# Optimization experiments

Hardware: AMD Instinct MI355X
Metric: run time of the kernel (lower is better)

Reference implementation:

```python
import jax, jax.numpy as jnp
import numpy as np

THRESH_FACTOR = 0.7


def ternarize(w):
    # w: [in_features, out_features]; per-row (dim 0) delta/alpha stats
    n = w.shape[1]
    abs_w = jnp.abs(w)
    delta = (THRESH_FACTOR / n) * abs_w.sum(axis=1, keepdims=True)  # [in, 1]
    mask = abs_w > delta
    count = mask.sum(axis=1, keepdims=True).astype(w.dtype)
    alpha = jnp.where(mask, abs_w, 0).sum(axis=1, keepdims=True) / count  # [in, 1]
    tern = jnp.where(w > delta, 1.0, jnp.where(w < -delta, -1.0, 0.0)).astype(w.dtype)
    return tern * alpha


def setup_inputs() -> dict:
    key = jax.random.key(0)
    k1, k2, k3 = jax.random.split(key, 3)
    B, IN, OUT = 8192, 4096, 4096
    x = jax.random.normal(k1, (B, IN), dtype=jnp.float32)
    # kaiming-uniform-ish then clamp to [-1, 1] as in the module
    bound_w = float(np.sqrt(6.0 / ((1.0 + 5.0) * IN)))
    weights = jax.random.uniform(k2, (IN, OUT), minval=-bound_w, maxval=bound_w, dtype=jnp.float32)
    weights = jnp.clip(weights, -1.0, 1.0)
    bound_b = 1.0 / float(np.sqrt(IN))
    bias = jax.random.uniform(k3, (OUT,), minval=-bound_b, maxval=bound_b, dtype=jnp.float32)
    return {"x": x, "weights": weights, "bias": bias}


def reference(x, weights, bias):
    w_t = ternarize(weights)
    return jnp.matmul(x, w_t) + bias
```

## Files before the change

### kernel.cpp

```cpp
#include <hip/hip_runtime.h>
#include <stdint.h>
#include <stddef.h>

#define IN_F 4096
#define OUT_F 4096

typedef int i32x4 __attribute__((ext_vector_type(4)));
typedef float f32x4 __attribute__((ext_vector_type(4)));


__device__ static inline void async16(const void* g, void* l) {
    __builtin_amdgcn_global_load_lds(
        (const __attribute__((address_space(1))) unsigned int*)g,
        (__attribute__((address_space(3))) unsigned int*)l,
        16, 0, 0);
}

__device__ static inline double wred_d(double v) {
#pragma unroll
    for (int o = 32; o > 0; o >>= 1) v += __shfl_down(v, o, 64);
    return v;
}

__device__ static inline int wred_i(int v) {
#pragma unroll
    for (int o = 32; o > 0; o >>= 1) v += __shfl_down(v, o, 64);
    return v;
}

__device__ static inline float wred_max(float v) {
#pragma unroll
    for (int o = 32; o > 0; o >>= 1) v = fmaxf(v, __shfl_down(v, o, 64));
    return v;
}


__global__ __launch_bounds__(256) void rowstats_tern_kernel(
    const float* __restrict__ w,
    float* __restrict__ alpha_o,
    int8_t* __restrict__ T) {
    __shared__ float rowbuf[OUT_F];
    __shared__ double sh_s[4], sh_m[4];
    __shared__ int sh_c[4];
    const int row = blockIdx.x;
    const int t = threadIdx.x;
    const int lane = t & 63, wv = t >> 6;
    const float4* wr = (const float4*)(w + (size_t)row * OUT_F);

    double s = 0.0;
#pragma unroll
    for (int it = 0; it < 4; ++it) {
        float4 v = wr[t + it * 256];
        ((float4*)rowbuf)[t + it * 256] = v;
        s += (double)fabsf(v.x) + (double)fabsf(v.y) +
             (double)fabsf(v.z) + (double)fabsf(v.w);
    }
    double sw = wred_d(s);
    if (lane == 0) sh_s[wv] = sw;
    __syncthreads();
    const double delta = (sh_s[0] + sh_s[1] + sh_s[2] + sh_s[3]) *
                         (0.7 / (double)OUT_F);

    int8_t* trow = T + (size_t)row * OUT_F;
    double ms = 0.0;
    int cnt = 0;
#pragma unroll
    for (int k = 0; k < 16; ++k) {
        float v = rowbuf[k * 256 + t];
        double a = (double)fabsf(v);
        if (a > delta) { ms += a; ++cnt; }
        int8_t q = 0;
        if ((double)v > delta)       q = 1;
        else if ((double)v < -delta) q = -1;
        trow[k * 256 + t] = q;
    }
    double msw = wred_d(ms);
    int cw = wred_i(cnt);
    if (lane == 0) { sh_m[wv] = msw; sh_c[wv] = cw; }
    __syncthreads();
    if (t == 0) {
        double mtot = sh_m[0] + sh_m[1] + sh_m[2] + sh_m[3];
        int ctot = sh_c[0] + sh_c[1] + sh_c[2] + sh_c[3];
        alpha_o[row] = (float)(mtot / (double)ctot);
    }
}


__global__ __launch_bounds__(256) void transpose_i8_kernel(
    const int8_t* __restrict__ T,
    int8_t* __restrict__ Tt) {
    __shared__ int8_t lds[64][72];
    const int t = threadIdx.x;
    const int i0 = blockIdx.y * 64;
    const int j0 = blockIdx.x * 64;

#pragma unroll
    for (int it = 0; it < 4; ++it) {
        int idx = it * 256 + t;
        int r = idx >> 4;
        int c4 = idx & 15;
        uchar4 v = *(const uchar4*)(T + (size_t)(i0 + r) * OUT_F + j0 + c4 * 4);
        lds[c4 * 4 + 0][r] = (int8_t)v.x;
        lds[c4 * 4 + 1][r] = (int8_t)v.y;
        lds[c4 * 4 + 2][r] = (int8_t)v.z;
        lds[c4 * 4 + 3][r] = (int8_t)v.w;
    }
    __syncthreads();
#pragma unroll
    for (int it = 0; it < 2; ++it) {
        int idx = it * 256 + t;
        int rr = idx >> 3;
        int cc = idx & 7;
        unsigned long long v = *(const unsigned long long*)&lds[rr][cc * 8];
        *(unsigned long long*)(Tt + (size_t)(j0 + rr) * IN_F + i0 + cc * 8) = v;
    }
}


__global__ __launch_bounds__(256) void xquant_kernel(
    const float* __restrict__ x,
    const float* __restrict__ alpha,
    int8_t* __restrict__ xq,
    float* __restrict__ scale_o) {
    __shared__ float rowbuf[IN_F];
    __shared__ float sh_mx[4];
    const int row = blockIdx.x;
    const int t = threadIdx.x;
    const int lane = t & 63, wv = t >> 6;
    const float4* xr = (const float4*)(x + (size_t)row * IN_F);
    const float4* ar = (const float4*)alpha;

    float mx = 0.0f;
#pragma unroll
    for (int it = 0; it < 4; ++it) {
        float4 v = xr[t + it * 256];
        float4 a = ar[t + it * 256];
        v.x *= a.x; v.y *= a.y; v.z *= a.z; v.w *= a.w;
        ((float4*)rowbuf)[t + it * 256] = v;
        mx = fmaxf(mx, fmaxf(fmaxf(fabsf(v.x), fabsf(v.y)),
                             fmaxf(fabsf(v.z), fabsf(v.w))));
    }
    float mw = wred_max(mx);
    if (lane == 0) sh_mx[wv] = mw;
    __syncthreads();
    const float rmax = fmaxf(fmaxf(sh_mx[0], sh_mx[1]), fmaxf(sh_mx[2], sh_mx[3]));
    const float inv = (rmax > 0.0f) ? (127.0f / rmax) : 0.0f;

    int8_t* qrow = xq + (size_t)row * IN_F;
#pragma unroll
    for (int k = 0; k < 16; ++k) {
        float v = rowbuf[k * 256 + t];
        qrow[k * 256 + t] = (int8_t)__float2int_rn(v * inv);
    }
    if (t == 0) scale_o[row] = (rmax > 0.0f) ? (rmax / 127.0f) : 1.0f;
}


__global__ __launch_bounds__(256) void gemm_i8_kernel(
    const int8_t* __restrict__ Xq,
    const int8_t* __restrict__ Tq,
    const float* __restrict__ scale,
    const float* __restrict__ bias,
    float* __restrict__ out) {
    __shared__ __align__(16) int8_t lds_a[128 * 64];
    __shared__ __align__(16) int8_t lds_b[128 * 64];
    const int K = IN_F;
    const int t = threadIdx.x;
    const int lane = t & 63;
    const int wave = t >> 6;
    const int m0 = blockIdx.y * 128;
    const int n0 = blockIdx.x * 128;

    const int r0 = t >> 2;
    const int cb = (t & 3) << 4;
    const int8_t* gA0 = Xq + (size_t)(m0 + r0) * K + cb;
    const int8_t* gA1 = Xq + (size_t)(m0 + r0 + 64) * K + cb;
    const int8_t* gB0 = Tq + (size_t)(n0 + r0) * K + cb;
    const int8_t* gB1 = Tq + (size_t)(n0 + r0 + 64) * K + cb;
    char* lA0 = (char*)lds_a + t * 16;
    char* lA1 = (char*)lds_a + t * 16 + 4096;
    char* lB0 = (char*)lds_b + t * 16;
    char* lB1 = (char*)lds_b + t * 16 + 4096;

    i32x4 acc[4][4];
#pragma unroll
    for (int i = 0; i < 4; ++i)
#pragma unroll
        for (int j = 0; j < 4; ++j)
#pragma unroll
            for (int r = 0; r < 4; ++r) acc[i][j][r] = 0;

    const int q16 = (lane >> 4) << 4;
    const int lm = lane & 15;
    const int wm = (wave >> 1) << 6;
    const int wn = (wave & 1) << 6;
    const int8_t* pa = lds_a + (wm + lm) * 64 + q16;
    const int8_t* pb = lds_b + (wn + lm) * 64 + q16;

    for (int k0 = 0; k0 < K; k0 += 64) {
        async16(gA0 + k0, lA0);
        async16(gA1 + k0, lA1);
        async16(gB0 + k0, lB0);
        async16(gB1 + k0, lB1);
        __syncthreads();
        i32x4 af[4], bf[4];
#pragma unroll
        for (int i = 0; i < 4; ++i) {
            af[i] = *(const i32x4*)(pa + i * 16 * 64);
            bf[i] = *(const i32x4*)(pb + i * 16 * 64);
        }
#pragma unroll
        for (int i = 0; i < 4; ++i)
#pragma unroll
            for (int j = 0; j < 4; ++j)
                acc[i][j] = __builtin_amdgcn_mfma_i32_16x16x64_i8(
                    af[i], bf[j], acc[i][j], 0, 0, 0);
        __syncthreads();
    }

    const int q4 = (lane >> 4) << 2;
#pragma unroll
    for (int i = 0; i < 4; ++i) {
        float sc[4];
#pragma unroll
        for (int r = 0; r < 4; ++r) sc[r] = scale[m0 + wm + i * 16 + q4 + r];
#pragma unroll
        for (int j = 0; j < 4; ++j) {
            int col = n0 + wn + j * 16 + lm;
            float b = bias[col];
#pragma unroll
            for (int r = 0; r < 4; ++r) {
                int row = m0 + wm + i * 16 + q4 + r;
                out[(size_t)row * OUT_F + col] =
                    (float)acc[i][j][r] * sc[r] + b;
            }
        }
    }
}


extern "C" void kernel_launch(void* const* d_in, const int* in_sizes, int n_in,
                              void* d_out, int out_size, void* d_ws, size_t ws_size,
                              hipStream_t stream) {
    const float* x = (const float*)d_in[0];
    const float* w = (const float*)d_in[1];
    const float* bias = (const float*)d_in[2];
    float* out = (float*)d_out;
    const int B = in_sizes[0] / IN_F;

    char* ws = (char*)d_ws;
    int8_t* Tt = (int8_t*)ws;
    int8_t* T = (int8_t*)(ws + (size_t)16777216);
    int8_t* Xq = (int8_t*)(ws + (size_t)16777216);
    float* alpha = (float*)(ws + (size_t)50331648);
    float* scale = (float*)(ws + (size_t)50331648 + 16384);

    rowstats_tern_kernel<<<IN_F, 256, 0, stream>>>(w, alpha, T);
    transpose_i8_kernel<<<dim3(OUT_F / 64, IN_F / 64), 256, 0, stream>>>(T, Tt);
    xquant_kernel<<<B, 256, 0, stream>>>(x, alpha, Xq, scale);
    gemm_i8_kernel<<<dim3(OUT_F / 128, B / 128), 256, 0, stream>>>(Xq, Tt, scale, bias, out);
}
```

Measured before the change: 441.8 us.

## Rewrite int8 GEMM as 256x256 tile, 8-wave, double-buffered phased pipeline

Replaces the 128x128 single-buffer int8 GEMM with a 256x256-tile, 512-thread kernel. It uses 128KB of dynamic LDS for double buffering, XOR-swizzled LDS layout to avoid bank conflicts, and an 8-phase schedule that interleaves async global->LDS loads with MFMA blocks under s_setprio. It also adds a grid swizzle for L2 locality. The aim is to hide memory latency and raise arithmetic intensity in the dominant GEMM, at the cost of high register/LDS use and hand-managed waitcnt/barrier correctness.

New measurement: 384.9 us. 1.15x faster.

```diff
diff --git a/kernel.cpp b/kernel.cpp
--- a/kernel.cpp
+++ b/kernel.cpp
@@ -156,83 +156,172 @@
 }
 
 
-__global__ __launch_bounds__(256) void gemm_i8_kernel(
+#define GBARRIER() asm volatile("s_barrier" ::: "memory")
+
+#define STAGE(G, GR0, TILE, LBASE, HALF)                                        \
+    do {                                                                        \
+        _Pragma("unroll")                                                       \
+        for (int rr_ = 0; rr_ < 2; ++rr_) {                                     \
+            const int L_ = (HALF) * 1024 + rr_ * 512 + t;                       \
+            const int row_ = L_ >> 3;                                           \
+            const int gch_ = (L_ & 7) ^ (row_ & 7);                             \
+            async16((G) + (size_t)((GR0) + row_) * IN_F + (TILE) * 128 +        \
+                        (gch_ << 4),                                            \
+                    (LBASE) + (L_ << 4));                                       \
+        }                                                                       \
+    } while (0)
+
+#define READ_A(BUF, MI0)                                                        \
+    _Pragma("unroll")                                                           \
+    for (int mi_ = 0; mi_ < 4; ++mi_) {                                         \
+        a[2 * mi_]     = *(const i32x4*)((BUF) + offA_k0 + ((MI0) + mi_) * 2048); \
+        a[2 * mi_ + 1] = *(const i32x4*)((BUF) + offA_k1 + ((MI0) + mi_) * 2048); \
+    }
+
+#define READ_B(BUF, NI0, DST)                                                   \
+    _Pragma("unroll")                                                           \
+    for (int ni_ = 0; ni_ < 2; ++ni_) {                                         \
+        DST[2 * ni_]     = *(const i32x4*)((BUF) + offB_k0 + ((NI0) + ni_) * 2048); \
+        DST[2 * ni_ + 1] = *(const i32x4*)((BUF) + offB_k1 + ((NI0) + ni_) * 2048); \
+    }
+
+#define MFMA_Q(MI0, NI0, BSRC)                                                  \
+    do {                                                                        \
+        __builtin_amdgcn_s_setprio(1);                                          \
+        _Pragma("unroll")                                                       \
+        for (int mi_ = 0; mi_ < 4; ++mi_) {                                     \
+            _Pragma("unroll")                                                   \
+            for (int ni_ = 0; ni_ < 2; ++ni_) {                                 \
+                acc[(MI0) + mi_][(NI0) + ni_] =                                 \
+                    __builtin_amdgcn_mfma_i32_16x16x64_i8(                      \
+                        a[2 * mi_], BSRC[2 * ni_],                              \
+                        acc[(MI0) + mi_][(NI0) + ni_], 0, 0, 0);                \
+                acc[(MI0) + mi_][(NI0) + ni_] =                                 \
+                    __builtin_amdgcn_mfma_i32_16x16x64_i8(                      \
+                        a[2 * mi_ + 1], BSRC[2 * ni_ + 1],                      \
+                        acc[(MI0) + mi_][(NI0) + ni_], 0, 0, 0);                \
+            }                                                                   \
+        }                                                                       \
+        __builtin_amdgcn_s_setprio(0);                                          \
+    } while (0)
+
+__global__ __launch_bounds__(512, 2) void gemm_i8_8ph(
     const int8_t* __restrict__ Xq,
     const int8_t* __restrict__ Tq,
     const float* __restrict__ scale,
     const float* __restrict__ bias,
     float* __restrict__ out) {
-    __shared__ __align__(16) int8_t lds_a[128 * 64];
-    __shared__ __align__(16) int8_t lds_b[128 * 64];
+    extern __shared__ __align__(16) int8_t lds[];
     const int K = IN_F;
+    const int NT = K / 128;
+    const int NI = NT / 2;
+
     const int t = threadIdx.x;
     const int lane = t & 63;
     const int wave = t >> 6;
-    const int m0 = blockIdx.y * 128;
-    const int n0 = blockIdx.x * 128;
-
-    const int r0 = t >> 2;
-    const int cb = (t & 3) << 4;
-    const int8_t* gA0 = Xq + (size_t)(m0 + r0) * K + cb;
-    const int8_t* gA1 = Xq + (size_t)(m0 + r0 + 64) * K + cb;
-    const int8_t* gB0 = Tq + (size_t)(n0 + r0) * K + cb;
-    const int8_t* gB1 = Tq + (size_t)(n0 + r0 + 64) * K + cb;
-    char* lA0 = (char*)lds_a + t * 16;
-    char* lA1 = (char*)lds_a + t * 16 + 4096;
-    char* lB0 = (char*)lds_b + t * 16;
-    char* lB1 = (char*)lds_b + t * 16 + 4096;
-
-    i32x4 acc[4][4];
-#pragma unroll
-    for (int i = 0; i < 4; ++i)
+    const int lm = lane & 15;
+    const int qh = lane >> 4;
+    const int wm = (wave >> 2) << 7;
+    const int wn = (wave & 3) << 6;
+
+    const int nwg = gridDim.x;
+    const int id = blockIdx.x;
+    const int swz = (id & 7) * (nwg >> 3) + (id >> 3);
+    const int m0 = (swz >> 4) << 8;
+    const int n0 = (swz & 15) << 8;
+
+    int8_t* const A0  = lds;
+    int8_t* const B0  = lds + 32768;
+    int8_t* const A1b = lds + 65536;
+    int8_t* const B1b = lds + 98304;
+
+    const int swzs = lm & 7;
+    const int offA_k0 = (wm + lm) * 128 + ((qh ^ swzs) << 4);
+    const int offA_k1 = (wm + lm) * 128 + (((4 + qh) ^ swzs) << 4);
+    const int offB_k0 = (wn + lm) * 128 + ((qh ^ swzs) << 4);
+    const int offB_k1 = (wn + lm) * 128 + (((4 + qh) ^ swzs) << 4);
+
+    i32x4 acc[8][4];
+#pragma unroll
+    for (int i = 0; i < 8; ++i)
 #pragma unroll
         for (int j = 0; j < 4; ++j)
 #pragma unroll
             for (int r = 0; r < 4; ++r) acc[i][j][r] = 0;
 
-    const int q16 = (lane >> 4) << 4;
-    const int lm = lane & 15;
-    const int wm = (wave >> 1) << 6;
-    const int wn = (wave & 1) << 6;
-    const int8_t* pa = lds_a + (wm + lm) * 64 + q16;
-    const int8_t* pb = lds_b + (wn + lm) * 64 + q16;
-
-    for (int k0 = 0; k0 < K; k0 += 64) {
-        async16(gA0 + k0, lA0);
-        async16(gA1 + k0, lA1);
-        async16(gB0 + k0, lB0);
-        async16(gB1 + k0, lB1);
-        __syncthreads();
-        i32x4 af[4], bf[4];
-#pragma unroll
-        for (int i = 0; i < 4; ++i) {
-            af[i] = *(const i32x4*)(pa + i * 16 * 64);
-            bf[i] = *(const i32x4*)(pb + i * 16 * 64);
-        }
-#pragma unroll
-        for (int i = 0; i < 4; ++i)
-#pragma unroll
-            for (int j = 0; j < 4; ++j)
-                acc[i][j] = __builtin_amdgcn_mfma_i32_16x16x64_i8(
-                    af[i], bf[j], acc[i][j], 0, 0, 0);
-        __syncthreads();
-    }
-
-    const int q4 = (lane >> 4) << 2;
-#pragma unroll
-    for (int i = 0; i < 4; ++i) {
+    i32x4 a[8], bA[4], bB[4];
+
+    STAGE(Xq, m0, 0, A0, 0);
+    STAGE(Xq, m0, 0, A0, 1);
+    STAGE(Tq, n0, 0, B0, 0);
+    STAGE(Tq, n0, 0, B0, 1);
+    STAGE(Xq, m0, 1, A1b, 0);
+    asm volatile("s_waitcnt vmcnt(2)" ::: "memory");
+    GBARRIER();
+
+#pragma unroll 1
+    for (int i = 0; i < NI; ++i) {
+        const int kt = 2 * i;
+        READ_A(A0, 0);
+        READ_B(B0, 0, bA);
+        STAGE(Xq, m0, kt + 1, A1b, 1);
+        GBARRIER();
+        MFMA_Q(0, 0, bA);
+        GBARRIER();
+        READ_B(B0, 2, bB);
+        STAGE(Tq, n0, kt + 1, B1b, 0);
+        GBARRIER();
+        MFMA_Q(0, 2, bB);
+        GBARRIER();
+        READ_A(A0, 4);
+        STAGE(Tq, n0, kt + 1, B1b, 1);
+        GBARRIER();
+        MFMA_Q(4, 0, bA);
+        GBARRIER();
+        if (kt + 2 < NT) STAGE(Xq, m0, kt + 2, A0, 0);
+        GBARRIER();
+        MFMA_Q(4, 2, bB);
+        if (i + 1 < NI) asm volatile("s_waitcnt vmcnt(2)" ::: "memory");
+        else            asm volatile("s_waitcnt vmcnt(0)" ::: "memory");
+        GBARRIER();
+        READ_A(A1b, 0);
+        READ_B(B1b, 0, bA);
+        if (kt + 2 < NT) STAGE(Xq, m0, kt + 2, A0, 1);
+        GBARRIER();
+        MFMA_Q(0, 0, bA);
+        GBARRIER();
+        READ_B(B1b, 2, bB);
+        if (kt + 2 < NT) STAGE(Tq, n0, kt + 2, B0, 0);
+        GBARRIER();
+        MFMA_Q(0, 2, bB);
+        GBARRIER();
+        READ_A(A1b, 4);
+        if (kt + 2 < NT) STAGE(Tq, n0, kt + 2, B0, 1);
+        GBARRIER();
+        MFMA_Q(4, 0, bA);
+        GBARRIER();
+        if (kt + 3 < NT) STAGE(Xq, m0, kt + 3, A1b, 0);
+        GBARRIER();
+        MFMA_Q(4, 2, bB);
+        if (i + 1 < NI) asm volatile("s_waitcnt vmcnt(2)" ::: "memory");
+        GBARRIER();
+    }
+
+    const int q4 = qh << 2;
+#pragma unroll
+    for (int mi = 0; mi < 8; ++mi) {
         float sc[4];
 #pragma unroll
-        for (int r = 0; r < 4; ++r) sc[r] = scale[m0 + wm + i * 16 + q4 + r];
-#pragma unroll
-        for (int j = 0; j < 4; ++j) {
-            int col = n0 + wn + j * 16 + lm;
+        for (int r = 0; r < 4; ++r) sc[r] = scale[m0 + wm + mi * 16 + q4 + r];
+#pragma unroll
+        for (int ni = 0; ni < 4; ++ni) {
+            int col = n0 + wn + ni * 16 + lm;
             float b = bias[col];
 #pragma unroll
             for (int r = 0; r < 4; ++r) {
-                int row = m0 + wm + i * 16 + q4 + r;
+                int row = m0 + wm + mi * 16 + q4 + r;
                 out[(size_t)row * OUT_F + col] =
-                    (float)acc[i][j][r] * sc[r] + b;
+                    (float)acc[mi][ni][r] * sc[r] + b;
             }
         }
     }
@@ -255,8 +344,16 @@
     float* alpha = (float*)(ws + (size_t)50331648);
     float* scale = (float*)(ws + (size_t)50331648 + 16384);
 
+    static int lds_set = 0;
+    if (!lds_set) {
+        hipFuncSetAttribute((const void*)gemm_i8_8ph,
+                            hipFuncAttributeMaxDynamicSharedMemorySize, 131072);
+        lds_set = 1;
+    }
+
     rowstats_tern_kernel<<<IN_F, 256, 0, stream>>>(w, alpha, T);
     transpose_i8_kernel<<<dim3(OUT_F / 64, IN_F / 64), 256, 0, stream>>>(T, Tt);
     xquant_kernel<<<B, 256, 0, stream>>>(x, alpha, Xq, scale);
-    gemm_i8_kernel<<<dim3(OUT_F / 128, B / 128), 256, 0, stream>>>(Xq, Tt, scale, bias, out);
-}
+    const int nwg = (B / 256) * (OUT_F / 256);
+    gemm_i8_8ph<<<dim3(nwg), dim3(512), 131072, stream>>>(Xq, Tt, scale, bias, out);
+}
```
